# Kernel tuning notes

Hardware: AMD Instinct MI355X
Metric: run time of the kernel (lower is better)

Reference implementation:

```python
import jax, jax.numpy as jnp
import numpy as np

E = 128
H = 4
D = E // H  # head dim = 32
NEG = -1e9


def setup_inputs() -> dict:
    key = jax.random.key(0)
    ks = jax.random.split(key, 4)
    B, N = 8, 2048
    x = jax.random.normal(ks[0], (B, N, E), dtype=jnp.float32)
    adj = jax.random.randint(ks[1], (B, N, N), 0, 2, dtype=jnp.int32)
    # nn.MultiheadAttention params: packed in_proj (3E,E) + out_proj (E,E)
    in_proj_w = jax.random.normal(ks[2], (3 * E, E), dtype=jnp.float32) * (1.0 / np.sqrt(E))
    in_proj_b = jnp.zeros((3 * E,), dtype=jnp.float32)
    out_w = jax.random.normal(ks[3], (E, E), dtype=jnp.float32) * (1.0 / np.sqrt(E))
    out_b = jnp.zeros((E,), dtype=jnp.float32)
    return {"x": x, "adj": adj, "in_proj_w": in_proj_w, "in_proj_b": in_proj_b,
            "out_w": out_w, "out_b": out_b}


def reference(x, adj, in_proj_w, in_proj_b, out_w, out_b):
    B, N, _ = x.shape
    # additive mask from FIRST batch element only (as in the torch module)
    mask = jnp.where(adj[0] == 0, jnp.float32(NEG), jnp.float32(0.0))  # (N,N)
    # packed QKV projection: x @ W^T + b
    qkv = x @ in_proj_w.T + in_proj_b  # (B,N,3E)
    q, k, v = jnp.split(qkv, 3, axis=-1)
    # (B,N,E) -> (B,H,N,D)
    def heads(t):
        return t.reshape(B, N, H, D).transpose(0, 2, 1, 3)
    q, k, v = heads(q), heads(k), heads(v)
    scores = jnp.einsum('bhnd,bhmd->bhnm', q, k) / jnp.sqrt(jnp.float32(D))
    scores = scores + mask[None, None]  # broadcast shared mask
    attn = jax.nn.softmax(scores, axis=-1)
    out = jnp.einsum('bhnm,bhmd->bhnd', attn, v)  # (B,H,N,D)
    out = out.transpose(0, 2, 1, 3).reshape(B, N, E)
    return out @ out_w.T + out_b
```

## Files before the change

kernel.cpp:

```cpp
#include <hip/hip_runtime.h>


#define EDIM 128
#define SCALE2 0.25503483f
#define COFF  -5.7707801f

typedef unsigned int uint32;
typedef float f32x4 __attribute__((ext_vector_type(4)));
typedef short s16x8 __attribute__((ext_vector_type(8)));
typedef _Float16 f16x2 __attribute__((ext_vector_type(2)));
typedef _Float16 f16x4 __attribute__((ext_vector_type(4)));
typedef _Float16 f16x8 __attribute__((ext_vector_type(8)));
typedef __fp16 g16x2 __attribute__((ext_vector_type(2)));

__device__ inline float bf2f(ushort u) { return __uint_as_float(((uint32)u) << 16); }
__device__ inline ushort f2bf(float f) {
  uint32 u = __float_as_uint(f);
  u += 0x7fffu + ((u >> 16) & 1u);
  return (ushort)(u >> 16);
}
__device__ inline uint32 packbf(float a, float b) {
  uint32 ua = __float_as_uint(a) + 0x8000u;
  uint32 ub = __float_as_uint(b) + 0x8000u;
  return __builtin_amdgcn_perm(ub, ua, 0x07060302u);
}
__device__ inline f16x2 pkrtz(float a, float b) {
  g16x2 t = __builtin_amdgcn_cvt_pkrtz(a, b);
  return __builtin_bit_cast(f16x2, t);
}
__device__ inline float fexp2(float x) {
#if __has_builtin(__builtin_amdgcn_exp2f)
  return __builtin_amdgcn_exp2f(x);
#else
  return __exp2f(x);
#endif
}

__device__ inline f32x4 mfma32(s16x8 a, s16x8 b, f32x4 c) {
  return __builtin_amdgcn_mfma_f32_16x16x32_bf16(a, b, c, 0, 0, 0);
}
__device__ inline f32x4 mfma32h(f16x8 a, f16x8 b, f32x4 c) {
  return __builtin_amdgcn_mfma_f32_16x16x32_f16(a, b, c, 0, 0, 0);
}

#if __has_builtin(__builtin_amdgcn_global_load_lds)
#define HAVE_GLL 1
__device__ inline void gll16(const void* g, void* l) {
  __builtin_amdgcn_global_load_lds(
      (const __attribute__((address_space(1))) unsigned int*)g,
      (__attribute__((address_space(3))) unsigned int*)l, 16, 0, 0);
}
#else
#define HAVE_GLL 0
#endif

__device__ inline int sniff_fp32(const ushort* __restrict__ xus) {
  int lane = threadIdx.x & 63, cnt = 0;
#pragma unroll
  for (int i = 0; i < 4; i++) {
    ushort v = xus[2 * (lane * 4 + i)];
    int ex = (v >> 7) & 0xFF;
    cnt += (ex >= 100 && ex <= 140) ? 1 : 0;
  }
#pragma unroll
  for (int s = 1; s < 64; s <<= 1) cnt += __shfl_xor(cnt, s);
  return cnt < 128;
}

__device__ inline s16x8 load8(const void* p, size_t e, int fp32) {
  if (fp32) {
    const float* f = (const float*)p + e;
    float4 lo = *(const float4*)f;
    float4 hi = *(const float4*)(f + 4);
    union { s16x8 s; uint32 u[4]; } r;
    r.u[0] = packbf(lo.x, lo.y);
    r.u[1] = packbf(lo.z, lo.w);
    r.u[2] = packbf(hi.x, hi.y);
    r.u[3] = packbf(hi.z, hi.w);
    return r.s;
  }
  return *(const s16x8*)((const ushort*)p + e);
}
__device__ inline float loads(const void* p, size_t e, int fp32) {
  return fp32 ? ((const float*)p)[e] : bf2f(((const ushort*)p)[e]);
}

__global__ __launch_bounds__(256) void k_pre(const void* __restrict__ x,
                                             const void* __restrict__ w,
                                             const void* __restrict__ bias,
                                             ushort* __restrict__ Qg,
                                             ushort* __restrict__ Kg,
                                             _Float16* __restrict__ Vth,
                                             const int4* __restrict__ adj4,
                                             uint32* __restrict__ mb) {
  if (blockIdx.y >= 6) {
    int g = ((blockIdx.y - 6) * 256 + blockIdx.x) * 256 + threadIdx.x;
    int4 v = adj4[g];
    int lane = threadIdx.x & 63;
    uint32 nib = (v.x != 0 ? 1u : 0u) | (v.y != 0 ? 2u : 0u) |
                 (v.z != 0 ? 4u : 0u) | (v.w != 0 ? 8u : 0u);
    uint32 wbit = nib << (4 * (lane & 7));
    wbit |= __shfl_xor(wbit, 1);
    wbit |= __shfl_xor(wbit, 2);
    wbit |= __shfl_xor(wbit, 4);
    if ((lane & 7) == 0) mb[g >> 3] = wbit;
    return;
  }

  const int fp32 = sniff_fp32((const ushort*)x);
  const int tid = threadIdx.x;
  const int wave = tid >> 6, lane = tid & 63, L = lane & 15, quad = lane >> 4;
  const int mt = blockIdx.x * 64 + wave * 16;
  const int jt0 = blockIdx.y * 4;

  s16x8 a[4];
#pragma unroll
  for (int ks = 0; ks < 4; ks++)
    a[ks] = load8(x, (size_t)(mt + L) * EDIM + ks * 32 + quad * 8, fp32);

  const int bidx = mt >> 11;
  const int npos0 = (mt & 2047) + quad * 4;

  for (int jj = 0; jj < 4; jj++) {
    int jt = jt0 + jj;
    f32x4 acc = {0.f, 0.f, 0.f, 0.f};
#pragma unroll
    for (int ks = 0; ks < 4; ks++) {
      s16x8 bf = load8(w, (size_t)(jt * 16 + L) * EDIM + ks * 32 + quad * 8, fp32);
      acc = mfma32(a[ks], bf, acc);
    }
    int j = jt * 16 + L;
    float badd = loads(bias, j, fp32);
    int jm = j & 127;
    int h = jm >> 5, d = jm & 31;
    int bh = bidx * 4 + h;
    int ch = npos0 >> 7, kk = npos0 & 127;
    if (jt < 8) {
#pragma unroll
      for (int r = 0; r < 4; r++)
        Qg[(size_t)bh * 65536 + (size_t)(npos0 + r) * 32 + d] = f2bf((acc[r] + badd) * SCALE2);
    } else if (jt < 16) {
      int sub = kk >> 5, k32 = kk & 31, t = k32 >> 3, r8 = k32 & 7;
      int slot0 = sub * 32 + ((r8 >> 2) << 4) + t * 4;
      size_t kb = (size_t)bh * 65536 + (size_t)ch * 4096;
#pragma unroll
      for (int r = 0; r < 4; r++)
        Kg[kb + (size_t)(slot0 + r) * 32 + (((d >> 3) ^ r) << 3) + (d & 7)] =
            f2bf(acc[r] + badd);
    } else {
      int g = kk >> 3, e0 = kk & 7;
      f16x2 h0 = pkrtz(acc[0] + badd, acc[1] + badd);
      f16x2 h1 = pkrtz(acc[2] + badd, acc[3] + badd);
      f16x4 pk; pk[0] = h0[0]; pk[1] = h0[1]; pk[2] = h1[0]; pk[3] = h1[1];
      *(f16x4*)(Vth + (size_t)bh * 65536 + (size_t)ch * 4096 + d * 128 +
                (g ^ (d & 7)) * 8 + e0) = pk;
    }
  }
}

__global__ __launch_bounds__(512) void k_attn(const ushort* __restrict__ Qg,
                                              const ushort* __restrict__ Kg,
                                              const _Float16* __restrict__ Vth,
                                              const uint32* __restrict__ mb,
                                              ushort* __restrict__ Oa) {
  __shared__ ushort Klds[2][2][128 * 32];
  __shared__ ushort Vlds[2][2][32 * 128];

  const int tid = threadIdx.x;
  const int wv = tid >> 6, lane = tid & 63, L = lane & 15, quad = lane >> 4;
  const int half = wv >> 2, wl = wv & 3;
  const int bh = blockIdx.x >> 4;
  const int q0 = (blockIdx.x & 15) * 128 + wl * 32;
  const int qgA = q0 + L, qgB = q0 + 16 + L;

  const ushort* Qb = Qg + (size_t)bh * 65536;
  s16x8 qfA = *(const s16x8*)(Qb + (size_t)qgA * 32 + quad * 8);
  s16x8 qfB = *(const s16x8*)(Qb + (size_t)qgB * 32 + quad * 8);

  f32x4 OA0 = {0,0,0,0}, OA1 = {0,0,0,0}, OB0 = {0,0,0,0}, OB1 = {0,0,0,0};
  f32x4 LA = {0,0,0,0}, LB = {0,0,0,0};
  f16x8 ones;
#pragma unroll
  for (int i = 0; i < 8; i++) ones[i] = (_Float16)1.0f;

  const char* Kg8 = (const char*)(Kg + (size_t)bh * 65536) + (size_t)half * 65536;
  const char* Vg8 = (const char*)(Vth + (size_t)bh * 65536) + (size_t)half * 65536;
  const int g0 = quad ^ (L & 3);

#define STAGE(cc, p)                                                          \
  do {                                                                        \
    _Pragma("unroll")                                                         \
    for (int j = 0; j < 2; j++) {                                             \
      int off = (wl + 4 * j) * 1024;                                          \
      gll16(Kg8 + (size_t)(cc) * 8192 + off + lane * 16,                      \
            (char*)Klds[half][p] + off);                                      \
      gll16(Vg8 + (size_t)(cc) * 8192 + off + lane * 16,                      \
            (char*)Vlds[half][p] + off);                                      \
    }                                                                         \
  } while (0)

#if HAVE_GLL
  STAGE(0, 0);
#else
  {
    int t256 = tid & 255;
#pragma unroll
    for (int r = 0; r < 2; r++) {
      int idx = r * 256 + t256;
      *(s16x8*)((char*)Klds[half][0] + idx * 16) = *(const s16x8*)(Kg8 + idx * 16);
      *(s16x8*)((char*)Vlds[half][0] + idx * 16) = *(const s16x8*)(Vg8 + idx * 16);
    }
  }
#endif

  for (int cc = 0; cc < 8; cc++) {
    const int p = cc & 1;
    __syncthreads();
#if HAVE_GLL
    if (cc + 1 < 8) STAGE(cc + 1, 1 - p);
#else
    if (cc + 1 < 8) {
      int t256 = tid & 255;
#pragma unroll
      for (int r = 0; r < 2; r++) {
        int idx = r * 256 + t256;
        *(s16x8*)((char*)Klds[half][1 - p] + idx * 16) =
            *(const s16x8*)(Kg8 + (size_t)(cc + 1) * 8192 + idx * 16);
        *(s16x8*)((char*)Vlds[half][1 - p] + idx * 16) =
            *(const s16x8*)(Vg8 + (size_t)(cc + 1) * 8192 + idx * 16);
      }
    }
#endif

    const int c = half * 8 + cc;
    uint4 mA = *(const uint4*)(mb + (size_t)qgA * 64 + c * 4);
    uint4 mB = *(const uint4*)(mb + (size_t)qgB * 64 + c * 4);
    uint32 mAw[4] = {mA.x, mA.y, mA.z, mA.w};
    uint32 mBw[4] = {mB.x, mB.y, mB.z, mB.w};

#pragma unroll
    for (int sub = 0; sub < 4; sub++) {
      const f32x4 Zc = {COFF, COFF, COFF, COFF};
      s16x8 kf0 = *(const s16x8*)&Klds[half][p][(sub * 32 + L) * 32 + g0 * 8];
      s16x8 kf1 = *(const s16x8*)&Klds[half][p][(sub * 32 + 16 + L) * 32 + g0 * 8];
      f32x4 sA0 = mfma32(kf0, qfA, Zc), sA1 = mfma32(kf1, qfA, Zc);
      f32x4 sB0 = mfma32(kf0, qfB, Zc), sB1 = mfma32(kf1, qfB, Zc);

      uint32 mwqA = mAw[sub] >> (quad * 8);
      uint32 mwqB = mBw[sub] >> (quad * 8);
      union { f16x8 v; f16x2 h[4]; } pA, pB;
      float a0 = ((mwqA >> 0) & 1u) ? fexp2(sA0[0]) : 0.f;
      float a1 = ((mwqA >> 1) & 1u) ? fexp2(sA0[1]) : 0.f;
      float a2 = ((mwqA >> 2) & 1u) ? fexp2(sA0[2]) : 0.f;
      float a3 = ((mwqA >> 3) & 1u) ? fexp2(sA0[3]) : 0.f;
      float a4 = ((mwqA >> 4) & 1u) ? fexp2(sA1[0]) : 0.f;
      float a5 = ((mwqA >> 5) & 1u) ? fexp2(sA1[1]) : 0.f;
      float a6 = ((mwqA >> 6) & 1u) ? fexp2(sA1[2]) : 0.f;
      float a7 = ((mwqA >> 7) & 1u) ? fexp2(sA1[3]) : 0.f;
      pA.h[0] = pkrtz(a0, a1); pA.h[1] = pkrtz(a2, a3);
      pA.h[2] = pkrtz(a4, a5); pA.h[3] = pkrtz(a6, a7);
      float b0 = ((mwqB >> 0) & 1u) ? fexp2(sB0[0]) : 0.f;
      float b1 = ((mwqB >> 1) & 1u) ? fexp2(sB0[1]) : 0.f;
      float b2 = ((mwqB >> 2) & 1u) ? fexp2(sB0[2]) : 0.f;
      float b3 = ((mwqB >> 3) & 1u) ? fexp2(sB0[3]) : 0.f;
      float b4 = ((mwqB >> 4) & 1u) ? fexp2(sB1[0]) : 0.f;
      float b5 = ((mwqB >> 5) & 1u) ? fexp2(sB1[1]) : 0.f;
      float b6 = ((mwqB >> 6) & 1u) ? fexp2(sB1[2]) : 0.f;
      float b7 = ((mwqB >> 7) & 1u) ? fexp2(sB1[3]) : 0.f;
      pB.h[0] = pkrtz(b0, b1); pB.h[1] = pkrtz(b2, b3);
      pB.h[2] = pkrtz(b4, b5); pB.h[3] = pkrtz(b6, b7);

      int g = (sub * 4 + quad) ^ (L & 7);
      f16x8 vf0 = *(const f16x8*)&Vlds[half][p][L * 128 + g * 8];
      f16x8 vf1 = *(const f16x8*)&Vlds[half][p][(16 + L) * 128 + g * 8];
      OA0 = mfma32h(vf0, pA.v, OA0);  OA1 = mfma32h(vf1, pA.v, OA1);
      OB0 = mfma32h(vf0, pB.v, OB0);  OB1 = mfma32h(vf1, pB.v, OB1);
      LA  = mfma32h(ones, pA.v, LA);  LB  = mfma32h(ones, pB.v, LB);
    }
  }

  __syncthreads();
  float* cb = (float*)&Klds[0][0][0];
  const int cbase = wl * 1088;
  if (half) {
#pragma unroll
    for (int r = 0; r < 4; r++) {
      cb[cbase + L * 33 + quad * 4 + r]             = OA0[r];
      cb[cbase + L * 33 + 16 + quad * 4 + r]        = OA1[r];
      cb[cbase + (16 + L) * 33 + quad * 4 + r]      = OB0[r];
      cb[cbase + (16 + L) * 33 + 16 + quad * 4 + r] = OB1[r];
    }
    if (quad == 0) {
      cb[cbase + 1056 + L]      = LA[0];
      cb[cbase + 1056 + 16 + L] = LB[0];
    }
  }
  __syncthreads();
  if (!half) {
#pragma unroll
    for (int r = 0; r < 4; r++) {
      OA0[r] += cb[cbase + L * 33 + quad * 4 + r];
      OA1[r] += cb[cbase + L * 33 + 16 + quad * 4 + r];
      OB0[r] += cb[cbase + (16 + L) * 33 + quad * 4 + r];
      OB1[r] += cb[cbase + (16 + L) * 33 + 16 + quad * 4 + r];
    }
    float rnA = 1.0f / (LA[0] + cb[cbase + 1056 + L]);
    float rnB = 1.0f / (LB[0] + cb[cbase + 1056 + 16 + L]);
    int b = bh >> 2, h = bh & 3;
    {
      size_t ob = ((size_t)(b * 2048 + qgA)) * 128 + h * 32 + quad * 4;
      ushort4 p0, p1;
      p0.x = f2bf(OA0[0] * rnA); p0.y = f2bf(OA0[1] * rnA);
      p0.z = f2bf(OA0[2] * rnA); p0.w = f2bf(OA0[3] * rnA);
      p1.x = f2bf(OA1[0] * rnA); p1.y = f2bf(OA1[1] * rnA);
      p1.z = f2bf(OA1[2] * rnA); p1.w = f2bf(OA1[3] * rnA);
      *(ushort4*)(Oa + ob) = p0; *(ushort4*)(Oa + ob + 16) = p1;
    }
    {
      size_t ob = ((size_t)(b * 2048 + qgB)) * 128 + h * 32 + quad * 4;
      ushort4 p0, p1;
      p0.x = f2bf(OB0[0] * rnB); p0.y = f2bf(OB0[1] * rnB);
      p0.z = f2bf(OB0[2] * rnB); p0.w = f2bf(OB0[3] * rnB);
      p1.x = f2bf(OB1[0] * rnB); p1.y = f2bf(OB1[1] * rnB);
      p1.z = f2bf(OB1[2] * rnB); p1.w = f2bf(OB1[3] * rnB);
      *(ushort4*)(Oa + ob) = p0; *(ushort4*)(Oa + ob + 16) = p1;
    }
  }
}

__global__ __launch_bounds__(256) void k_proj(void* outp, const ushort* Oa,
                                              const void* w, const void* bias,
                                              const ushort* __restrict__ xus) {
  const int fp32 = sniff_fp32(xus);
  const ushort* src = Oa;
  const int tid = threadIdx.x;
  const int wave = tid >> 6, lane = tid & 63, L = lane & 15, quad = lane >> 4;
  const int mt = blockIdx.x * 64 + wave * 16;
  const int jt0 = blockIdx.y * 2;

  s16x8 a[4];
#pragma unroll
  for (int ks = 0; ks < 4; ks++)
    a[ks] = *(const s16x8*)(src + (size_t)(mt + L) * EDIM + ks * 32 + quad * 8);

  for (int jt = jt0; jt < jt0 + 2; jt++) {
    f32x4 acc = {0.f, 0.f, 0.f, 0.f};
#pragma unroll
    for (int ks = 0; ks < 4; ks++) {
      s16x8 bf = load8(w, (size_t)(jt * 16 + L) * EDIM + ks * 32 + quad * 8, fp32);
      acc = mfma32(a[ks], bf, acc);
    }
    float badd = loads(bias, jt * 16 + L, fp32);
#pragma unroll
    for (int r = 0; r < 4; r++) {
      size_t idx = (size_t)(mt + quad * 4 + r) * EDIM + jt * 16 + L;
      if (fp32) ((float*)outp)[idx] = acc[r] + badd;
      else      ((ushort*)outp)[idx] = f2bf(acc[r] + badd);
    }
  }
}

extern "C" void kernel_launch(void* const* d_in, const int* in_sizes, int n_in,
                              void* d_out, int out_size, void* d_ws, size_t ws_size,
                              hipStream_t stream) {
  const void* x   = d_in[0];
  const int*  adj = (const int*)d_in[1];
  const void* ipw = d_in[2];
  const void* ipb = d_in[3];
  const void* ow  = d_in[4];
  const void* ob  = d_in[5];

  char* ws = (char*)d_ws;
  ushort*   Qg  = (ushort*)(ws);
  ushort*   Kg  = (ushort*)(ws + ((size_t)4 << 20));
  _Float16* Vth = (_Float16*)(ws + ((size_t)8 << 20));
  uint32*   mb  = (uint32*)(ws + ((size_t)12 << 20));
  ushort*   Oa  = (ushort*)(ws + ((size_t)13 << 20));

  hipLaunchKernelGGL(k_pre, dim3(256, 22), dim3(256), 0, stream, x, ipw, ipb,
                     Qg, Kg, Vth, (const int4*)adj, mb);
  hipLaunchKernelGGL(k_attn, dim3(512), dim3(512), 0, stream, Qg, Kg, Vth, mb,
                     Oa);
  hipLaunchKernelGGL(k_proj, dim3(256, 4), dim3(256), 0, stream, d_out, Oa, ow, ob,
                     (const ushort*)x);
}
```

Measured before the change: 247.3 us.

## Fuse output projection into attention kernel via last-block atomic counter

Drops the separate k_proj launch. Each attention block bumps a per-(batch, query-tile) atomic counter, and the fourth block to finish (the last of the four heads) runs the output projection for that 128-row tile. The counter is zeroed in k_pre. The goal is to remove one kernel launch and its inter-kernel gap, at the cost of fences, atomics and serial tail work done by only a quarter of the blocks. It also adds a launch_bounds min-blocks hint of 4 on k_attn, which may change register allocation.

```diff
diff --git a/kernel.cpp b/kernel.cpp
--- a/kernel.cpp
+++ b/kernel.cpp
@@ -92,8 +92,11 @@
                                              ushort* __restrict__ Kg,
                                              _Float16* __restrict__ Vth,
                                              const int4* __restrict__ adj4,
-                                             uint32* __restrict__ mb) {
+                                             uint32* __restrict__ mb,
+                                             uint32* __restrict__ cnt) {
   if (blockIdx.y >= 6) {
+    if (blockIdx.y == 6 && blockIdx.x == 0 && threadIdx.x < 128)
+      cnt[threadIdx.x] = 0;
     int g = ((blockIdx.y - 6) * 256 + blockIdx.x) * 256 + threadIdx.x;
     int4 v = adj4[g];
     int lane = threadIdx.x & 63;
@@ -158,13 +161,19 @@
   }
 }
 
-__global__ __launch_bounds__(512) void k_attn(const ushort* __restrict__ Qg,
-                                              const ushort* __restrict__ Kg,
-                                              const _Float16* __restrict__ Vth,
-                                              const uint32* __restrict__ mb,
-                                              ushort* __restrict__ Oa) {
+__global__ __launch_bounds__(512, 4) void k_attn(const ushort* __restrict__ Qg,
+                                                 const ushort* __restrict__ Kg,
+                                                 const _Float16* __restrict__ Vth,
+                                                 const uint32* __restrict__ mb,
+                                                 ushort* __restrict__ Oa,
+                                                 void* __restrict__ outp,
+                                                 const void* __restrict__ ow,
+                                                 const void* __restrict__ obias,
+                                                 const ushort* __restrict__ xus,
+                                                 uint32* __restrict__ cnt) {
   __shared__ ushort Klds[2][2][128 * 32];
   __shared__ ushort Vlds[2][2][32 * 128];
+  __shared__ int lastflag;
 
   const int tid = threadIdx.x;
   const int wv = tid >> 6, lane = tid & 63, L = lane & 15, quad = lane >> 4;
@@ -326,31 +335,33 @@
       *(ushort4*)(Oa + ob) = p0; *(ushort4*)(Oa + ob + 16) = p1;
     }
   }
-}
-
-__global__ __launch_bounds__(256) void k_proj(void* outp, const ushort* Oa,
-                                              const void* w, const void* bias,
-                                              const ushort* __restrict__ xus) {
+
+  __syncthreads();
+  if (tid == 0) {
+    __threadfence();
+    int g = (int)(bh >> 2) * 16 + (int)(blockIdx.x & 15);
+    lastflag = (atomicAdd(&cnt[g], 1u) == 3u) ? 1 : 0;
+  }
+  __syncthreads();
+  if (!lastflag) return;
+  __threadfence();
+
   const int fp32 = sniff_fp32(xus);
-  const ushort* src = Oa;
-  const int tid = threadIdx.x;
-  const int wave = tid >> 6, lane = tid & 63, L = lane & 15, quad = lane >> 4;
-  const int mt = blockIdx.x * 64 + wave * 16;
-  const int jt0 = blockIdx.y * 2;
+  const int mt = (int)(bh >> 2) * 2048 + (int)(blockIdx.x & 15) * 128 + wv * 16;
 
   s16x8 a[4];
 #pragma unroll
   for (int ks = 0; ks < 4; ks++)
-    a[ks] = *(const s16x8*)(src + (size_t)(mt + L) * EDIM + ks * 32 + quad * 8);
-
-  for (int jt = jt0; jt < jt0 + 2; jt++) {
+    a[ks] = *(const s16x8*)(Oa + (size_t)(mt + L) * EDIM + ks * 32 + quad * 8);
+
+  for (int jt = 0; jt < 8; jt++) {
     f32x4 acc = {0.f, 0.f, 0.f, 0.f};
 #pragma unroll
     for (int ks = 0; ks < 4; ks++) {
-      s16x8 bf = load8(w, (size_t)(jt * 16 + L) * EDIM + ks * 32 + quad * 8, fp32);
+      s16x8 bf = load8(ow, (size_t)(jt * 16 + L) * EDIM + ks * 32 + quad * 8, fp32);
       acc = mfma32(a[ks], bf, acc);
     }
-    float badd = loads(bias, jt * 16 + L, fp32);
+    float badd = loads(obias, jt * 16 + L, fp32);
 #pragma unroll
     for (int r = 0; r < 4; r++) {
       size_t idx = (size_t)(mt + quad * 4 + r) * EDIM + jt * 16 + L;
@@ -376,11 +387,10 @@
   _Float16* Vth = (_Float16*)(ws + ((size_t)8 << 20));
   uint32*   mb  = (uint32*)(ws + ((size_t)12 << 20));
   ushort*   Oa  = (ushort*)(ws + ((size_t)13 << 20));
+  uint32*   cnt = (uint32*)(ws + ((size_t)17 << 20));
 
   hipLaunchKernelGGL(k_pre, dim3(256, 22), dim3(256), 0, stream, x, ipw, ipb,
-                     Qg, Kg, Vth, (const int4*)adj, mb);
+                     Qg, Kg, Vth, (const int4*)adj, mb, cnt);
   hipLaunchKernelGGL(k_attn, dim3(512), dim3(512), 0, stream, Qg, Kg, Vth, mb,
-                     Oa);
-  hipLaunchKernelGGL(k_proj, dim3(256, 4), dim3(256), 0, stream, d_out, Oa, ow, ob,
-                     (const ushort*)x);
-}
+                     Oa, d_out, ow, ob, (const ushort*)x, cnt);
+}
```

New measurement: 298.9 us. 1.21x slower.

## Read K/V fragments directly from global memory instead of LDS staging

Applied to the files above, without the earlier changes.

Removes the double-buffered LDS staging of K and V tiles, including the global_load_lds path and the per-chunk __syncthreads, and has each wave load its MFMA K/V fragments straight from global memory, relying on L1/L2 for reuse. LDS use shrinks to a small buffer used only for the final cross-half reduction. Launch bounds now request a minimum of 4 blocks per CU, to raise occupancy and hide global latency. The cost is redundant global/L2 traffic, because all four query waves in a half reload the same K/V, and the loads are no longer prefetched ahead of use.

```diff
diff --git a/kernel.cpp b/kernel.cpp
--- a/kernel.cpp
+++ b/kernel.cpp
@@ -42,17 +42,6 @@
 __device__ inline f32x4 mfma32h(f16x8 a, f16x8 b, f32x4 c) {
   return __builtin_amdgcn_mfma_f32_16x16x32_f16(a, b, c, 0, 0, 0);
 }
-
-#if __has_builtin(__builtin_amdgcn_global_load_lds)
-#define HAVE_GLL 1
-__device__ inline void gll16(const void* g, void* l) {
-  __builtin_amdgcn_global_load_lds(
-      (const __attribute__((address_space(1))) unsigned int*)g,
-      (__attribute__((address_space(3))) unsigned int*)l, 16, 0, 0);
-}
-#else
-#define HAVE_GLL 0
-#endif
 
 __device__ inline int sniff_fp32(const ushort* __restrict__ xus) {
   int lane = threadIdx.x & 63, cnt = 0;
@@ -158,13 +147,12 @@
   }
 }
 
-__global__ __launch_bounds__(512) void k_attn(const ushort* __restrict__ Qg,
-                                              const ushort* __restrict__ Kg,
-                                              const _Float16* __restrict__ Vth,
-                                              const uint32* __restrict__ mb,
-                                              ushort* __restrict__ Oa) {
-  __shared__ ushort Klds[2][2][128 * 32];
-  __shared__ ushort Vlds[2][2][32 * 128];
+__global__ __launch_bounds__(512, 4) void k_attn(const ushort* __restrict__ Qg,
+                                                 const ushort* __restrict__ Kg,
+                                                 const _Float16* __restrict__ Vth,
+                                                 const uint32* __restrict__ mb,
+                                                 ushort* __restrict__ Oa) {
+  __shared__ float cb[4352];
 
   const int tid = threadIdx.x;
   const int wv = tid >> 6, lane = tid & 63, L = lane & 15, quad = lane >> 4;
@@ -187,62 +175,23 @@
   const char* Vg8 = (const char*)(Vth + (size_t)bh * 65536) + (size_t)half * 65536;
   const int g0 = quad ^ (L & 3);
 
-#define STAGE(cc, p)                                                          \
-  do {                                                                        \
-    _Pragma("unroll")                                                         \
-    for (int j = 0; j < 2; j++) {                                             \
-      int off = (wl + 4 * j) * 1024;                                          \
-      gll16(Kg8 + (size_t)(cc) * 8192 + off + lane * 16,                      \
-            (char*)Klds[half][p] + off);                                      \
-      gll16(Vg8 + (size_t)(cc) * 8192 + off + lane * 16,                      \
-            (char*)Vlds[half][p] + off);                                      \
-    }                                                                         \
-  } while (0)
-
-#if HAVE_GLL
-  STAGE(0, 0);
-#else
-  {
-    int t256 = tid & 255;
-#pragma unroll
-    for (int r = 0; r < 2; r++) {
-      int idx = r * 256 + t256;
-      *(s16x8*)((char*)Klds[half][0] + idx * 16) = *(const s16x8*)(Kg8 + idx * 16);
-      *(s16x8*)((char*)Vlds[half][0] + idx * 16) = *(const s16x8*)(Vg8 + idx * 16);
-    }
-  }
-#endif
+  const char* kA = Kg8 + L * 64 + g0 * 16;
+  const char* vA = Vg8 + L * 256;
 
   for (int cc = 0; cc < 8; cc++) {
-    const int p = cc & 1;
-    __syncthreads();
-#if HAVE_GLL
-    if (cc + 1 < 8) STAGE(cc + 1, 1 - p);
-#else
-    if (cc + 1 < 8) {
-      int t256 = tid & 255;
-#pragma unroll
-      for (int r = 0; r < 2; r++) {
-        int idx = r * 256 + t256;
-        *(s16x8*)((char*)Klds[half][1 - p] + idx * 16) =
-            *(const s16x8*)(Kg8 + (size_t)(cc + 1) * 8192 + idx * 16);
-        *(s16x8*)((char*)Vlds[half][1 - p] + idx * 16) =
-            *(const s16x8*)(Vg8 + (size_t)(cc + 1) * 8192 + idx * 16);
-      }
-    }
-#endif
-
     const int c = half * 8 + cc;
     uint4 mA = *(const uint4*)(mb + (size_t)qgA * 64 + c * 4);
     uint4 mB = *(const uint4*)(mb + (size_t)qgB * 64 + c * 4);
     uint32 mAw[4] = {mA.x, mA.y, mA.z, mA.w};
     uint32 mBw[4] = {mB.x, mB.y, mB.z, mB.w};
+    const char* kc = kA + (size_t)cc * 8192;
+    const char* vc = vA + (size_t)cc * 8192;
 
 #pragma unroll
     for (int sub = 0; sub < 4; sub++) {
       const f32x4 Zc = {COFF, COFF, COFF, COFF};
-      s16x8 kf0 = *(const s16x8*)&Klds[half][p][(sub * 32 + L) * 32 + g0 * 8];
-      s16x8 kf1 = *(const s16x8*)&Klds[half][p][(sub * 32 + 16 + L) * 32 + g0 * 8];
+      s16x8 kf0 = *(const s16x8*)(kc + sub * 2048);
+      s16x8 kf1 = *(const s16x8*)(kc + sub * 2048 + 1024);
       f32x4 sA0 = mfma32(kf0, qfA, Zc), sA1 = mfma32(kf1, qfA, Zc);
       f32x4 sB0 = mfma32(kf0, qfB, Zc), sB1 = mfma32(kf1, qfB, Zc);
 
@@ -271,8 +220,8 @@
       pB.h[2] = pkrtz(b4, b5); pB.h[3] = pkrtz(b6, b7);
 
       int g = (sub * 4 + quad) ^ (L & 7);
-      f16x8 vf0 = *(const f16x8*)&Vlds[half][p][L * 128 + g * 8];
-      f16x8 vf1 = *(const f16x8*)&Vlds[half][p][(16 + L) * 128 + g * 8];
+      f16x8 vf0 = *(const f16x8*)(vc + g * 16);
+      f16x8 vf1 = *(const f16x8*)(vc + 4096 + g * 16);
       OA0 = mfma32h(vf0, pA.v, OA0);  OA1 = mfma32h(vf1, pA.v, OA1);
       OB0 = mfma32h(vf0, pB.v, OB0);  OB1 = mfma32h(vf1, pB.v, OB1);
       LA  = mfma32h(ones, pA.v, LA);  LB  = mfma32h(ones, pB.v, LB);
@@ -280,7 +229,6 @@
   }
 
   __syncthreads();
-  float* cb = (float*)&Klds[0][0][0];
   const int cbase = wl * 1088;
   if (half) {
 #pragma unroll
```

Result: no change. 248.4 us (+0.4%).
